# Performance work log

Measured on AMD Instinct MI355X. Metric: run time of the kernel, lower is better.

The kernel has to match this reference:

```python
import jax, jax.numpy as jnp
import numpy as np

EPS = 1e-9
NUM_CLASSES = 10


def setup_inputs() -> dict:
    key = jax.random.key(0)
    k1, k2, k3, k4 = jax.random.split(key, 4)
    B, N, D = 1024, 16384, 512
    bound = 1.0 / (D ** 0.5)
    return {
        "x": jax.random.normal(k1, (B, D), dtype=jnp.float32),
        "ex_feats": jax.random.normal(k2, (N, D), dtype=jnp.float32),
        "ex_labels": jax.random.randint(k3, (N,), 0, NUM_CLASSES),
        "w_unconstrained": jax.random.uniform(k4, (D,), dtype=jnp.float32, minval=-bound, maxval=bound),
        "gamma_unconstrained": jnp.asarray(1.0, dtype=jnp.float32),
        "beta_unconstrained": jnp.asarray(1.0, dtype=jnp.float32),
    }


def reference(x, ex_feats, ex_labels, w_unconstrained, gamma_unconstrained, beta_unconstrained):
    # Constrained parameters
    beta = jax.nn.softplus(beta_unconstrained) + EPS      # scalar
    gamma = jax.nn.softplus(gamma_unconstrained) + EPS    # scalar
    w = jax.nn.softmax(w_unconstrained) + EPS             # (D,), positive, ~sums to 1

    # Weighted squared distance via quadratic (GEMM) expansion:
    # d[b,n] = sum_k w_k * (x[b,k] - e[n,k])^2
    #        = (x^2 @ w)[b] + (e^2 @ w)[n] - 2 * ((x*w) @ e^T)[b,n]
    x2w = (x * x) @ w                                     # (B,)
    e2w = (ex_feats * ex_feats) @ w                       # (N,)
    cross = (x * w[None, :]) @ ex_feats.T                 # (B, N) GEMM
    d = x2w[:, None] + e2w[None, :] - 2.0 * cross         # (B, N)

    sim = jnp.exp(-beta * d)                              # (B, N)

    # Scatter-add sim by class label -> class_sum (B, C).
    # With small C this is a dense GEMM against a one-hot matrix.
    onehot = jax.nn.one_hot(ex_labels, NUM_CLASSES, dtype=sim.dtype)  # (N, C)
    class_sum = sim @ onehot                              # (B, C)

    logits = gamma * jnp.log(class_sum + EPS)
    return logits
```

## Files before the change

### kernel.cpp

```cpp
#include <hip/hip_runtime.h>
#include <hip/hip_bf16.h>
#include <cstdint>


typedef __attribute__((ext_vector_type(4))) float f32x4;
typedef __attribute__((ext_vector_type(8))) __bf16 bf16x8;
typedef __attribute__((ext_vector_type(4))) _Float16 half4;
typedef __attribute__((ext_vector_type(4))) unsigned int u32x4;

#define DDIM 512
#define NC 10
#define NCP 16
#define NECH 64
#define EPSF 1e-9f

typedef const __attribute__((address_space(1))) void* gas_ptr;
typedef __attribute__((address_space(3))) void* las_ptr;

__device__ inline void async16(const void* g, void* l) {
  __builtin_amdgcn_global_load_lds((gas_ptr)g, (las_ptr)l, 16, 0, 0);
}

__device__ inline unsigned short f2bf(float f) {
  unsigned int u = __float_as_uint(f);
  u += 0x7FFFu + ((u >> 16) & 1u);
  return (unsigned short)(u >> 16);
}

__device__ inline float wave_sum(float v) {
  #pragma unroll
  for (int o = 32; o > 0; o >>= 1) v += __shfl_xor(v, o, 64);
  return v;
}

__device__ inline float softplus(float x) {
  return (x > 20.0f) ? x : log1pf(__expf(x));
}

__global__ void prep_w(const float* __restrict__ wu, const float* __restrict__ gu,
                       const float* __restrict__ bu, float* __restrict__ w,
                       float* __restrict__ scal) {
  __shared__ float sm[16];
  int t = threadIdx.x, lane = t & 63, wd = t >> 6;
  float v = wu[t];
  float m = v;
  #pragma unroll
  for (int o = 32; o > 0; o >>= 1) m = fmaxf(m, __shfl_xor(m, o, 64));
  if (lane == 0) sm[wd] = m;
  __syncthreads();
  float mm = sm[0];
  #pragma unroll
  for (int i = 1; i < 8; ++i) mm = fmaxf(mm, sm[i]);
  float e = __expf(v - mm);
  float s = wave_sum(e);
  if (lane == 0) sm[8 + wd] = s;
  __syncthreads();
  float ss = 0.f;
  #pragma unroll
  for (int i = 0; i < 8; ++i) ss += sm[8 + i];
  w[t] = e / ss + EPSF;
  if (t == 0) {
    scal[0] = softplus(bu[0]) + EPSF;
    scal[1] = softplus(gu[0]) + EPSF;
  }
}

__global__ void prep_rows(const float* __restrict__ in, const float* __restrict__ w,
                          unsigned short* __restrict__ obf, float* __restrict__ osq,
                          int mulw) {
  int lane = threadIdx.x & 63, wd = threadIdx.x >> 6;
  size_t row = (size_t)blockIdx.x * 4 + wd;
  const float* p = in + row * DDIM + lane * 8;
  const float* pw = w + lane * 8;
  float4 va = *(const float4*)(p);
  float4 vb = *(const float4*)(p + 4);
  float4 wa = *(const float4*)(pw);
  float4 wb = *(const float4*)(pw + 4);
  float s = va.x * va.x * wa.x + va.y * va.y * wa.y + va.z * va.z * wa.z + va.w * va.w * wa.w
          + vb.x * vb.x * wb.x + vb.y * vb.y * wb.y + vb.z * vb.z * wb.z + vb.w * vb.w * wb.w;
  unsigned short o[8];
  if (mulw) {
    o[0] = f2bf(va.x * wa.x); o[1] = f2bf(va.y * wa.y);
    o[2] = f2bf(va.z * wa.z); o[3] = f2bf(va.w * wa.w);
    o[4] = f2bf(vb.x * wb.x); o[5] = f2bf(vb.y * wb.y);
    o[6] = f2bf(vb.z * wb.z); o[7] = f2bf(vb.w * wb.w);
  } else {
    o[0] = f2bf(va.x); o[1] = f2bf(va.y); o[2] = f2bf(va.z); o[3] = f2bf(va.w);
    o[4] = f2bf(vb.x); o[5] = f2bf(vb.y); o[6] = f2bf(vb.z); o[7] = f2bf(vb.w);
  }
  u32x4 pk;
  pk[0] = (unsigned)o[0] | ((unsigned)o[1] << 16);
  pk[1] = (unsigned)o[2] | ((unsigned)o[3] << 16);
  pk[2] = (unsigned)o[4] | ((unsigned)o[5] << 16);
  pk[3] = (unsigned)o[6] | ((unsigned)o[7] << 16);
  *(u32x4*)(obf + row * DDIM + lane * 8) = pk;
  s = wave_sum(s);
  if (lane == 0) osq[row] = s;
}

__global__ __launch_bounds__(512, 2) void gemm_fused(
    const unsigned short* __restrict__ Ebf, const unsigned short* __restrict__ Xbf,
    const int* __restrict__ labels, const float* __restrict__ x2w,
    const float* __restrict__ e2w, const float* __restrict__ scal,
    float* __restrict__ part) {
  __shared__ __attribute__((aligned(16))) unsigned short smem[2 * 2 * 16384];
  __shared__ int lab[256];
  const int tid = threadIdx.x, lane = tid & 63, wid = tid >> 6;

  const int orig = blockIdx.x;
  const int xcd = orig & 7;
  const int local = orig >> 3;
  const int be = xcd * 8 + (local >> 2);
  const int bb = local & 3;

  if (tid < 256) lab[tid] = labels[be * 256 + tid];

  const unsigned short* srcE[4];
  const unsigned short* srcX[4];
  int loff[4];
  #pragma unroll
  for (int c = 0; c < 4; ++c) {
    int i = c * 512 + tid;
    int row = i >> 3, ch = i & 7;
    int sch = ch ^ (row & 7);
    srcE[c] = Ebf + (size_t)(be * 256 + row) * DDIM + sch * 8;
    srcX[c] = Xbf + (size_t)(bb * 256 + row) * DDIM + sch * 8;
    loff[c] = i * 8;
  }

  const int WE = (wid >> 2) * 128;
  const int WB = (wid & 3) * 64;

  int eoff[2][8], xoff[2][4];
  #pragma unroll
  for (int ks = 0; ks < 2; ++ks) {
    int ch = ks * 4 + (lane >> 4);
    #pragma unroll
    for (int f = 0; f < 8; ++f) {
      int erow = WE + f * 16 + (lane & 15);
      eoff[ks][f] = erow * 128 + ((ch ^ (erow & 7)) * 16);
    }
    #pragma unroll
    for (int f = 0; f < 4; ++f) {
      int xrow = WB + f * 16 + (lane & 15);
      xoff[ks][f] = xrow * 128 + ((ch ^ (xrow & 7)) * 16);
    }
  }

  #pragma unroll
  for (int c = 0; c < 4; ++c) {
    async16(srcE[c], &smem[loff[c]]);
    async16(srcX[c], &smem[16384 + loff[c]]);
    srcE[c] += 64; srcX[c] += 64;
  }
  __syncthreads();

  f32x4 acc[8][4] = {};
  int cur = 0;
  for (int kt = 0; kt < 8; ++kt) {
    if (kt < 7) {
      const int nb = (cur ^ 1) * 32768;
      #pragma unroll
      for (int c = 0; c < 4; ++c) {
        async16(srcE[c], &smem[nb + loff[c]]);
        async16(srcX[c], &smem[nb + 16384 + loff[c]]);
        srcE[c] += 64; srcX[c] += 64;
      }
    }
    const char* base = (const char*)&smem[cur * 32768];
    #pragma unroll
    for (int ks = 0; ks < 2; ++ks) {
      bf16x8 ef[8], xf[4];
      #pragma unroll
      for (int f = 0; f < 8; ++f) ef[f] = *(const bf16x8*)(base + eoff[ks][f]);
      #pragma unroll
      for (int f = 0; f < 4; ++f) xf[f] = *(const bf16x8*)(base + 32768 + xoff[ks][f]);
      #pragma unroll
      for (int fe = 0; fe < 8; ++fe)
        #pragma unroll
        for (int fb = 0; fb < 4; ++fb)
          acc[fe][fb] = __builtin_amdgcn_mfma_f32_16x16x32_bf16(ef[fe], xf[fb], acc[fe][fb], 0, 0, 0);
    }
    __syncthreads();
    cur ^= 1;
  }

  const float beta = scal[0];
  const int rb = (lane >> 4) * 4;
  const int col = lane & 15;
  float e2v[8][4];
  #pragma unroll
  for (int fe = 0; fe < 8; ++fe)
    #pragma unroll
    for (int r = 0; r < 4; ++r)
      e2v[fe][r] = e2w[be * 256 + WE + fe * 16 + rb + r];
  half4 oh[8];
  #pragma unroll
  for (int fe = 0; fe < 8; ++fe)
    #pragma unroll
    for (int i = 0; i < 4; ++i)
      oh[fe][i] = (lab[WE + fe * 16 + rb + i] == col) ? (_Float16)1.0f : (_Float16)0.0f;

  f32x4 csv[4];
  #pragma unroll
  for (int fb = 0; fb < 4; ++fb) {
    const float xv = x2w[bb * 256 + WB + fb * 16 + col];
    f32x4 cs = {0.f, 0.f, 0.f, 0.f};
    #pragma unroll
    for (int fe = 0; fe < 8; ++fe) {
      half4 sa;
      #pragma unroll
      for (int r = 0; r < 4; ++r)
        sa[r] = (_Float16)__expf(-beta * (xv + e2v[fe][r] - 2.0f * acc[fe][fb][r]));
      cs = __builtin_amdgcn_mfma_f32_16x16x16f16(sa, oh[fe], cs, 0, 0, 0);
    }
    csv[fb] = cs;
  }

  float* red = (float*)smem;
  const int half = WE >> 7;
  #pragma unroll
  for (int fb = 0; fb < 4; ++fb)
    #pragma unroll
    for (int r = 0; r < 4; ++r)
      red[(((half << 8) | (WB + fb * 16 + rb + r)) << 4) | col] = csv[fb][r];
  __syncthreads();

  {
    const int o = tid * 8;
    const int rl = o >> 4;
    const int c0 = o & 15;
    const float4* p0 = (const float4*)&red[(rl << 4) | c0];
    const float4* p1 = (const float4*)&red[((256 | rl) << 4) | c0];
    float4 a0 = p0[0], a1 = p0[1], b0 = p1[0], b1 = p1[1];
    float4 r0 = {a0.x + b0.x, a0.y + b0.y, a0.z + b0.z, a0.w + b0.w};
    float4 r1 = {a1.x + b1.x, a1.y + b1.y, a1.z + b1.z, a1.w + b1.w};
    float* g = &part[(((size_t)(bb * 256 + rl)) * NECH + be) * NCP + c0];
    *(float4*)g = r0;
    *(float4*)(g + 4) = r1;
  }
}

__global__ __launch_bounds__(256) void reduce_logits(
    const float* __restrict__ part, const float* __restrict__ scal,
    float* __restrict__ out) {
  const int lane = threadIdx.x & 63, wd = threadIdx.x >> 6;
  const int b = blockIdx.x * 4 + wd;
  const int cl = lane & 15, ch0 = lane >> 4;
  const float* p = part + (size_t)b * NECH * NCP;
  float v = 0.f;
  #pragma unroll
  for (int k = 0; k < 16; ++k)
    v += p[(ch0 + 4 * k) * NCP + cl];
  v += __shfl_xor(v, 16, 64);
  v += __shfl_xor(v, 32, 64);
  if (lane < NC) out[b * NC + lane] = scal[1] * logf(v + EPSF);
}

extern "C" void kernel_launch(void* const* d_in, const int* in_sizes, int n_in,
                              void* d_out, int out_size, void* d_ws, size_t ws_size,
                              hipStream_t stream) {
  const float* x  = (const float*)d_in[0];
  const float* ex = (const float*)d_in[1];
  const int* labels = (const int*)d_in[2];
  const float* wu = (const float*)d_in[3];
  const float* gu = (const float*)d_in[4];
  const float* bu = (const float*)d_in[5];
  float* out = (float*)d_out;
  const int B = in_sizes[0] / DDIM;
  const int N = in_sizes[2];

  char* ws = (char*)d_ws;
  const size_t off_scal = 0;
  const size_t off_w    = 256;
  const size_t off_x2w  = 4096;
  const size_t off_e2w  = off_x2w + (size_t)B * 4;
  const size_t off_xbf  = off_e2w + (size_t)N * 4;
  const size_t off_ebf  = off_xbf + (size_t)B * DDIM * 2;
  const size_t off_part = off_ebf + (size_t)N * DDIM * 2;
  const size_t need     = off_part + (size_t)B * NECH * NCP * 4;
  if (ws_size < need) return;

  float* scal = (float*)(ws + off_scal);
  float* w    = (float*)(ws + off_w);
  float* x2w  = (float*)(ws + off_x2w);
  float* e2w  = (float*)(ws + off_e2w);
  unsigned short* xbf = (unsigned short*)(ws + off_xbf);
  unsigned short* ebf = (unsigned short*)(ws + off_ebf);
  float* part = (float*)(ws + off_part);

  prep_w<<<1, DDIM, 0, stream>>>(wu, gu, bu, w, scal);
  prep_rows<<<B / 4, 256, 0, stream>>>(x, w, xbf, x2w, 1);
  prep_rows<<<N / 4, 256, 0, stream>>>(ex, w, ebf, e2w, 0);
  gemm_fused<<<(N / 256) * (B / 256), 512, 0, stream>>>(ebf, xbf, labels, x2w, e2w, scal, part);
  reduce_logits<<<B / 4, 256, 0, stream>>>(part, scal, out);
}
```

Baseline: 43.46 us.

## Interleave async loads with quarter-tile MFMA phases and merge prep launches

The GEMM main loop is split into four quarter phases. Each phase issues one chunk of the next tile's async global-to-LDS loads, reads LDS fragments, then runs a block of MFMAs under raised wave priority, with raw s_barrier separating the phases. This aims to hide global load latency and LDS reads behind matrix math instead of issuing all prefetches up front. It also merges the two prep_rows launches into one kernel that handles both x and ex rows, saving a launch. It adds many barriers per k-iteration and relies on a manual vmcnt wait, which is fragile for correctness.

```diff
diff --git a/kernel.cpp b/kernel.cpp
--- a/kernel.cpp
+++ b/kernel.cpp
@@ -13,6 +13,9 @@
 #define NCP 16
 #define NECH 64
 #define EPSF 1e-9f
+
+#define BAR()    asm volatile("s_barrier" ::: "memory")
+#define WAITV0() asm volatile("s_waitcnt vmcnt(0)" ::: "memory")
 
 typedef const __attribute__((address_space(1))) void* gas_ptr;
 typedef __attribute__((address_space(3))) void* las_ptr;
@@ -65,11 +68,19 @@
   }
 }
 
-__global__ void prep_rows(const float* __restrict__ in, const float* __restrict__ w,
-                          unsigned short* __restrict__ obf, float* __restrict__ osq,
-                          int mulw) {
+__global__ void prep_rows2(const float* __restrict__ x, const float* __restrict__ ex,
+                           const float* __restrict__ w,
+                           unsigned short* __restrict__ xbf, unsigned short* __restrict__ ebf,
+                           float* __restrict__ x2w, float* __restrict__ e2w, int nxb) {
   int lane = threadIdx.x & 63, wd = threadIdx.x >> 6;
-  size_t row = (size_t)blockIdx.x * 4 + wd;
+  const float* in; unsigned short* obf; float* osq; int mulw; size_t row;
+  if (blockIdx.x < (unsigned)nxb) {
+    in = x; obf = xbf; osq = x2w; mulw = 1;
+    row = (size_t)blockIdx.x * 4 + wd;
+  } else {
+    in = ex; obf = ebf; osq = e2w; mulw = 0;
+    row = (size_t)(blockIdx.x - nxb) * 4 + wd;
+  }
   const float* p = in + row * DDIM + lane * 8;
   const float* pw = w + lane * 8;
   float4 va = *(const float4*)(p);
@@ -131,19 +142,18 @@
   const int WE = (wid >> 2) * 128;
   const int WB = (wid & 3) * 64;
 
-  int eoff[2][8], xoff[2][4];
-  #pragma unroll
-  for (int ks = 0; ks < 2; ++ks) {
-    int ch = ks * 4 + (lane >> 4);
+  int eoff[8], xoff[4];
+  {
+    const int ch = lane >> 4;
     #pragma unroll
     for (int f = 0; f < 8; ++f) {
       int erow = WE + f * 16 + (lane & 15);
-      eoff[ks][f] = erow * 128 + ((ch ^ (erow & 7)) * 16);
+      eoff[f] = erow * 128 + ((ch ^ (erow & 7)) * 16);
     }
     #pragma unroll
     for (int f = 0; f < 4; ++f) {
       int xrow = WB + f * 16 + (lane & 15);
-      xoff[ks][f] = xrow * 128 + ((ch ^ (xrow & 7)) * 16);
+      xoff[f] = xrow * 128 + ((ch ^ (xrow & 7)) * 16);
     }
   }
 
@@ -157,33 +167,103 @@
 
   f32x4 acc[8][4] = {};
   int cur = 0;
+
+#define DSE(F, KS) (*(const bf16x8*)(bE + (eoff[F] ^ ((KS) << 6))))
+#define DSX(F, KS) (*(const bf16x8*)(bX + (xoff[F] ^ ((KS) << 6))))
+#define MFMA(A, B, C) __builtin_amdgcn_mfma_f32_16x16x32_bf16((A), (B), (C), 0, 0, 0)
+
   for (int kt = 0; kt < 8; ++kt) {
+    const int nb = (cur ^ 1) * 32768;
+    const char* bE = (const char*)smem + cur * 65536;
+    const char* bX = bE + 32768;
+    bf16x8 ef[4][2], xf[2][2];
+
+    #pragma unroll
+    for (int f = 0; f < 4; ++f) { ef[f][0] = DSE(f, 0); ef[f][1] = DSE(f, 1); }
+    #pragma unroll
+    for (int f = 0; f < 2; ++f) { xf[f][0] = DSX(f, 0); xf[f][1] = DSX(f, 1); }
     if (kt < 7) {
-      const int nb = (cur ^ 1) * 32768;
-      #pragma unroll
-      for (int c = 0; c < 4; ++c) {
-        async16(srcE[c], &smem[nb + loff[c]]);
-        async16(srcX[c], &smem[nb + 16384 + loff[c]]);
-        srcE[c] += 64; srcX[c] += 64;
-      }
-    }
-    const char* base = (const char*)&smem[cur * 32768];
-    #pragma unroll
-    for (int ks = 0; ks < 2; ++ks) {
-      bf16x8 ef[8], xf[4];
-      #pragma unroll
-      for (int f = 0; f < 8; ++f) ef[f] = *(const bf16x8*)(base + eoff[ks][f]);
-      #pragma unroll
-      for (int f = 0; f < 4; ++f) xf[f] = *(const bf16x8*)(base + 32768 + xoff[ks][f]);
-      #pragma unroll
-      for (int fe = 0; fe < 8; ++fe)
+      async16(srcE[0], &smem[nb + loff[0]]);
+      async16(srcX[0], &smem[nb + 16384 + loff[0]]);
+      srcE[0] += 64; srcX[0] += 64;
+    }
+    BAR();
+    __builtin_amdgcn_s_setprio(1);
+    #pragma unroll
+    for (int ks = 0; ks < 2; ++ks)
+      #pragma unroll
+      for (int fe = 0; fe < 4; ++fe)
         #pragma unroll
-        for (int fb = 0; fb < 4; ++fb)
-          acc[fe][fb] = __builtin_amdgcn_mfma_f32_16x16x32_bf16(ef[fe], xf[fb], acc[fe][fb], 0, 0, 0);
-    }
-    __syncthreads();
+        for (int fb = 0; fb < 2; ++fb)
+          acc[fe][fb] = MFMA(ef[fe][ks], xf[fb][ks], acc[fe][fb]);
+    __builtin_amdgcn_s_setprio(0);
+    BAR();
+
+    #pragma unroll
+    for (int f = 0; f < 2; ++f) { xf[f][0] = DSX(2 + f, 0); xf[f][1] = DSX(2 + f, 1); }
+    if (kt < 7) {
+      async16(srcE[1], &smem[nb + loff[1]]);
+      async16(srcX[1], &smem[nb + 16384 + loff[1]]);
+      srcE[1] += 64; srcX[1] += 64;
+    }
+    BAR();
+    __builtin_amdgcn_s_setprio(1);
+    #pragma unroll
+    for (int ks = 0; ks < 2; ++ks)
+      #pragma unroll
+      for (int fe = 0; fe < 4; ++fe)
+        #pragma unroll
+        for (int fb = 0; fb < 2; ++fb)
+          acc[fe][2 + fb] = MFMA(ef[fe][ks], xf[fb][ks], acc[fe][2 + fb]);
+    __builtin_amdgcn_s_setprio(0);
+    BAR();
+
+    #pragma unroll
+    for (int f = 0; f < 4; ++f) { ef[f][0] = DSE(4 + f, 0); ef[f][1] = DSE(4 + f, 1); }
+    #pragma unroll
+    for (int f = 0; f < 2; ++f) { xf[f][0] = DSX(f, 0); xf[f][1] = DSX(f, 1); }
+    if (kt < 7) {
+      async16(srcE[2], &smem[nb + loff[2]]);
+      async16(srcX[2], &smem[nb + 16384 + loff[2]]);
+      srcE[2] += 64; srcX[2] += 64;
+    }
+    BAR();
+    __builtin_amdgcn_s_setprio(1);
+    #pragma unroll
+    for (int ks = 0; ks < 2; ++ks)
+      #pragma unroll
+      for (int fe = 0; fe < 4; ++fe)
+        #pragma unroll
+        for (int fb = 0; fb < 2; ++fb)
+          acc[4 + fe][fb] = MFMA(ef[fe][ks], xf[fb][ks], acc[4 + fe][fb]);
+    __builtin_amdgcn_s_setprio(0);
+    BAR();
+
+    #pragma unroll
+    for (int f = 0; f < 2; ++f) { xf[f][0] = DSX(2 + f, 0); xf[f][1] = DSX(2 + f, 1); }
+    if (kt < 7) {
+      async16(srcE[3], &smem[nb + loff[3]]);
+      async16(srcX[3], &smem[nb + 16384 + loff[3]]);
+      srcE[3] += 64; srcX[3] += 64;
+    }
+    BAR();
+    __builtin_amdgcn_s_setprio(1);
+    #pragma unroll
+    for (int ks = 0; ks < 2; ++ks)
+      #pragma unroll
+      for (int fe = 0; fe < 4; ++fe)
+        #pragma unroll
+        for (int fb = 0; fb < 2; ++fb)
+          acc[4 + fe][2 + fb] = MFMA(ef[fe][ks], xf[fb][ks], acc[4 + fe][2 + fb]);
+    __builtin_amdgcn_s_setprio(0);
+
+    WAITV0();
+    BAR();
     cur ^= 1;
   }
+#undef DSE
+#undef DSX
+#undef MFMA
 
   const float beta = scal[0];
   const int rb = (lane >> 4) * 4;
@@ -217,6 +297,7 @@
     csv[fb] = cs;
   }
 
+  __syncthreads();
   float* red = (float*)smem;
   const int half = WE >> 7;
   #pragma unroll
@@ -290,8 +371,7 @@
   float* part = (float*)(ws + off_part);
 
   prep_w<<<1, DDIM, 0, stream>>>(wu, gu, bu, w, scal);
-  prep_rows<<<B / 4, 256, 0, stream>>>(x, w, xbf, x2w, 1);
-  prep_rows<<<N / 4, 256, 0, stream>>>(ex, w, ebf, e2w, 0);
+  prep_rows2<<<(B + N) / 4, 256, 0, stream>>>(x, ex, w, xbf, ebf, x2w, e2w, B / 4);
   gemm_fused<<<(N / 256) * (B / 256), 512, 0, stream>>>(ebf, xbf, labels, x2w, e2w, scal, part);
   reduce_logits<<<B / 4, 256, 0, stream>>>(part, scal, out);
 }
```

After: 43.68 us. About the same (+0.5%).
